# Kernel optimization log

Measured on AMD Instinct MI355X. Metric: run time of the kernel, lower is better.

The kernel has to match this reference:

```python
import jax, jax.numpy as jnp
import numpy as np
import math

B, T, C, H, W = 2, 3, 256, 64, 64   # batch, frames(=n_levels), d_model, feature H/W
M, P = 8, 4                          # n_heads, n_points
DH = C // M                          # dim per head


def conv2d(x, w, b):
    # 3x3 same-padded NCHW conv
    y = jax.lax.conv_general_dilated(x, w, (1, 1), 'SAME',
                                     dimension_numbers=('NCHW', 'OIHW', 'NCHW'))
    return y + b[None, :, None, None]


def setup_inputs() -> dict:
    key = jax.random.key(0)
    ks = jax.random.split(key, 10)
    query = jax.random.normal(ks[0], (B, T, C, H, W), jnp.float32)
    input_flatten = jax.random.normal(ks[1], (B, T, C, H, W), jnp.float32)
    reference_points = jax.random.uniform(ks[2], (B, H * W, T, 2), jnp.float32)
    input_spatial_shapes = jnp.tile(jnp.array([[H, W]], jnp.int32), (T, 1))
    input_level_start_index = jnp.arange(T, dtype=jnp.int32) * (H * W)
    input_padding_mask = jnp.zeros((B, T * H * W), bool)
    flow_forward = jax.random.normal(ks[3], (B, 2, 2, H, W), jnp.float32) * 2.0
    flow_backward = jax.random.normal(ks[4], (B, 2, 2, H, W), jnp.float32) * 2.0
    # conv params
    w_value = jax.random.normal(ks[5], (C, C, 3, 3), jnp.float32) * 0.02
    b_value = jnp.zeros((C,), jnp.float32)
    w_off = jax.random.normal(ks[6], (M * T * P * 2, T * C, 3, 3), jnp.float32) * 1e-3
    # sampling_offsets bias: ring of unit directions scaled by point index (as in _reset_parameters)
    thetas = jnp.arange(M, dtype=jnp.float32) * (2.0 * math.pi / M)
    grid = jnp.stack([jnp.cos(thetas), jnp.sin(thetas)], -1)
    grid = grid / jnp.max(jnp.abs(grid), -1, keepdims=True)
    grid = jnp.tile(grid.reshape(M, 1, 1, 2), (1, T, P, 1)) \
        * (jnp.arange(P, dtype=jnp.float32) + 1.0)[None, None, :, None]
    b_off = grid.reshape(-1)
    w_attn = jax.random.normal(ks[7], (M * T * P, T * C, 3, 3), jnp.float32) * 1e-3
    b_attn = jnp.zeros((M * T * P,), jnp.float32)
    w_out = jax.random.normal(ks[8], (C, C, 3, 3), jnp.float32) * 0.02
    b_out = jnp.zeros((C,), jnp.float32)
    return dict(query=query, reference_points=reference_points, input_flatten=input_flatten,
                input_spatial_shapes=input_spatial_shapes,
                input_level_start_index=input_level_start_index,
                input_padding_mask=input_padding_mask,
                flow_forward=flow_forward, flow_backward=flow_backward,
                w_value=w_value, b_value=b_value, w_off=w_off, b_off=b_off,
                w_attn=w_attn, b_attn=b_attn, w_out=w_out, b_out=b_out)


def ms_deform_attn(value, loc, attn):
    # value: (B, T*H*W, M, DH); loc in [0,1]: (B, Lq, M, T, P, 2); attn: (B, Lq, M, T, P)
    Lq = loc.shape[1]
    val = value.reshape(B, T, H * W, M, DH).transpose(0, 1, 3, 2, 4)  # (B,T,M,HW,DH)
    # grid_sample semantics, align_corners=False, zero padding
    x = loc[..., 0] * W - 0.5
    y = loc[..., 1] * H - 0.5
    x0 = jnp.floor(x); y0 = jnp.floor(y)
    wx = x - x0; wy = y - y0
    x0i = x0.astype(jnp.int32); y0i = y0.astype(jnp.int32)

    def tr(a):  # (B,Lq,M,T,P) -> (B,T,M,Lq*P)
        return jnp.transpose(a, (0, 3, 2, 1, 4)).reshape(B, T, M, Lq * P)

    acc = jnp.zeros((B, T, M, Lq * P, DH), value.dtype)
    for dx, dy, wgt in ((0, 0, (1 - wx) * (1 - wy)), (1, 0, wx * (1 - wy)),
                        (0, 1, (1 - wx) * wy), (1, 1, wx * wy)):
        ix = x0i + dx; iy = y0i + dy
        valid = (ix >= 0) & (ix < W) & (iy >= 0) & (iy < H)
        idx = tr(jnp.clip(iy, 0, H - 1) * W + jnp.clip(ix, 0, W - 1))
        g = jnp.take_along_axis(val, idx[..., None], axis=3)  # (B,T,M,Lq*P,DH)
        acc = acc + g * tr(wgt * valid)[..., None]
    acc = acc.reshape(B, T, M, Lq, P, DH)
    return jnp.einsum('ntmqpd,nqmtp->nqmd', acc, attn).reshape(B, Lq, M * DH)


def reference(query, reference_points, input_flatten, input_spatial_shapes,
              input_level_start_index, input_padding_mask, flow_forward, flow_backward,
              w_value, b_value, w_off, b_off, w_attn, b_attn, w_out, b_out):
    bs, t, c, h, w = query.shape
    value = conv2d(input_flatten.reshape(bs * t, c, h, w), w_value, b_value).reshape(bs, t, c, h, w)
    off = conv2d(query.reshape(bs, t * c, h, w), w_off, b_off)    # (bs, M*T*P*2, h, w)
    attn = conv2d(query.reshape(bs, t * c, h, w), w_attn, b_attn)  # (bs, M*T*P, h, w)

    # flatten to (bs, t*h*w, c) as in torch: flatten(3).transpose(2,3)
    value = value.reshape(bs, t, c, h * w).transpose(0, 1, 3, 2).reshape(bs, t * h * w, c)
    value = jnp.where(input_padding_mask[..., None], 0.0, value)
    value = value.reshape(bs, t * h * w, M, c // M)

    off = off.reshape(bs, -1, h * w).transpose(0, 2, 1).reshape(bs, h * w, M, t, P, 2)
    # flow-guided offsets: level 0 <- backward flow(1->0), level 1 <- zero, level 2 <- forward flow(1->2)
    flow_stack = jnp.stack([flow_backward[:, 0], jnp.zeros_like(flow_forward[:, 1]),
                            flow_forward[:, 1]], axis=2)            # (bs,2,t,h,w)
    flow = flow_stack.reshape(bs, 2, t, h * w).transpose(0, 3, 2, 1)  # (bs,hw,t,2)
    off = off + flow[:, :, None, :, None, :]

    attn = attn.reshape(bs, -1, h * w).transpose(0, 2, 1).reshape(bs, h * w, M, t * P)
    attn = jax.nn.softmax(attn, -1).reshape(bs, h * w, M, t, P)

    normalizer = jnp.stack([input_spatial_shapes[:, 1], input_spatial_shapes[:, 0]], -1).astype(off.dtype)
    loc = reference_points[:, :, None, :, None, :] + off / normalizer[None, None, None, :, None, :]

    out = ms_deform_attn(value, loc, attn)               # (bs, hw, c)
    out = out.reshape(bs, h, w, c).transpose(0, 3, 1, 2)  # (bs, c, h, w)
    return conv2d(out, w_out, b_out)
```

## Files before the change

kernel.cpp:

```cpp
#include <hip/hip_runtime.h>


#define HW_SZ 4096

typedef __attribute__((ext_vector_type(8))) short short8;
typedef __attribute__((ext_vector_type(4))) float f32x4;

__device__ __forceinline__ unsigned short f2bf(float f) {
    union { float f; unsigned u; } v; v.f = f;
    unsigned u = v.u;
    unsigned r = (u + 0x7FFFu + ((u >> 16) & 1u)) >> 16;
    return (unsigned short)r;
}
__device__ __forceinline__ float bf2f(unsigned short h) {
    union { unsigned u; float f; } v; v.u = ((unsigned)h) << 16;
    return v.f;
}

__device__ __forceinline__ void gld16(const void* g, void* l) {
    __builtin_amdgcn_global_load_lds(
        (const __attribute__((address_space(1))) unsigned*)g,
        (__attribute__((address_space(3))) unsigned*)l, 16, 0, 0);
}

__device__ __forceinline__ void repack2(
    int g, const float* __restrict__ w0, const float* __restrict__ w1,
    int split, int Cout, int Cin, unsigned short* __restrict__ out, int OBp)
{
    int lg = g & 3; int rest = g >> 2;
    int KB = Cin >> 5;
    int kb = rest % KB; int oc = rest / KB;
    int ob = oc >> 4, l16 = oc & 15;
    if (oc >= Cout) {
        uint4 z; z.x = z.y = z.z = z.w = 0u;
        #pragma unroll
        for (int tap = 0; tap < 9; ++tap)
            *(uint4*)(out + (((size_t)tap * OBp + ob) * KB + kb) * 512 + (lg * 16 + l16) * 8) = z;
        return;
    }
    const float* src = (oc < split)
        ? (w0 + ((size_t)oc * Cin + kb * 32 + lg * 8) * 9)
        : (w1 + ((size_t)(oc - split) * Cin + kb * 32 + lg * 8) * 9);
    float v[8][9];
    #pragma unroll
    for (int i = 0; i < 8; ++i)
        #pragma unroll
        for (int t = 0; t < 9; ++t)
            v[i][t] = src[i * 9 + t];
    #pragma unroll
    for (int tap = 0; tap < 9; ++tap) {
        unsigned p[4];
        #pragma unroll
        for (int j = 0; j < 4; ++j)
            p[j] = (unsigned)f2bf(v[2 * j][tap]) | ((unsigned)f2bf(v[2 * j + 1][tap]) << 16);
        uint4 o; o.x = p[0]; o.y = p[1]; o.z = p[2]; o.w = p[3];
        *(uint4*)(out + (((size_t)tap * OBp + ob) * KB + kb) * 512 + (lg * 16 + l16) * 8) = o;
    }
}

__global__ __launch_bounds__(256) void prep_fused(
    const float* __restrict__ vin_src, const float* __restrict__ qin_src,
    unsigned short* __restrict__ vdst, unsigned short* __restrict__ qdst,
    const float* __restrict__ w_value, const float* __restrict__ w_off,
    const float* __restrict__ w_attn, const float* __restrict__ w_out,
    const float* __restrict__ b_off, const float* __restrict__ b_attn,
    unsigned short* __restrict__ wpk_v, unsigned short* __restrict__ wpk_q,
    unsigned short* __restrict__ wpk_o, float* __restrict__ qbias,
    float* __restrict__ zbuf)
{
    int bid = blockIdx.x;
    if (bid < 6144) {
        int y = bid & 63, z = bid >> 6;
        const float* in; unsigned short* out; int Cin, img, kb;
        if (z < 48) { img = z >> 3; kb = z & 7; in = vin_src; out = vdst; Cin = 256; }
        else { int h = z - 48; img = h / 24; kb = h % 24; in = qin_src; out = qdst; Cin = 768; }
        __shared__ float s[32][65];
        int t = threadIdx.x;
        int x = t & 63, ic4 = t >> 6;
        const float* ip = in + ((size_t)img * Cin + kb * 32) * HW_SZ + y * 64;
        #pragma unroll
        for (int i = 0; i < 8; ++i) {
            int icl = ic4 * 8 + i;
            s[icl][x] = ip[(size_t)icl * HW_SZ + x];
        }
        __syncthreads();
        int p = t >> 2, h4 = t & 3;
        unsigned v[4];
        #pragma unroll
        for (int j = 0; j < 4; ++j) {
            unsigned lo = f2bf(s[h4 * 8 + 2 * j][p]);
            unsigned hi = f2bf(s[h4 * 8 + 2 * j + 1][p]);
            v[j] = lo | (hi << 16);
        }
        uint4 o; o.x = v[0]; o.y = v[1]; o.z = v[2]; o.w = v[3];
        *(uint4*)(out + ((size_t)img * HW_SZ + y * 64 + p) * Cin + kb * 32 + h4 * 8) = o;
    } else {
        int g = (bid - 6144) * 256 + threadIdx.x;
        if (g < 8192) {
            repack2(g, w_value, w_value, 256, 256, 256, wpk_v, 16);
        } else if (g < 45056) {
            repack2(g - 8192, w_off, w_attn, 192, 288, 768, wpk_q, 24);
        } else if (g < 53248) {
            repack2(g - 45056, w_out, w_out, 256, 256, 256, wpk_o, 16);
        } else {
            int i = g - 53248;
            if (i < 16) zbuf[i] = 0.f;
            if (i < 384) {
                float v = 0.f;
                if (i < 192) v = b_off[i]; else if (i < 288) v = b_attn[i - 192];
                qbias[i] = v;
            }
        }
    }
}

__device__ __forceinline__ void conv_core(
    const unsigned short* __restrict__ gin,
    const unsigned short* __restrict__ wpk,
    const float* __restrict__ bias,
    const unsigned short* __restrict__ zbuf,
    void* __restrict__ outp,
    int Cin, int KB, int OBp, int Cout, int mb, int y0, int outmode, int img,
    unsigned short* sbuf)
{
    const int tid = threadIdx.x;
    const int wv = tid >> 6, lane = tid & 63;
    const int l16 = lane & 15, lg = lane >> 4;
    const int obBase = mb * 8 + wv * 2;

    const unsigned short* sptr[4];
    int okk[4];
    #pragma unroll
    for (int i = 0; i < 4; ++i) {
        int ii = 4 * i + wv;
        int r = ii * 64 + lane;
        sptr[i] = zbuf; okk[i] = 0;
        if (ii < 13 && r < 792) {
            int rr = r / 264;
            int rem = r - rr * 264;
            int icg = rem / 66;
            int cc = rem - icg * 66;
            int gy = y0 - 1 + rr, gx = cc - 1;
            if ((unsigned)gy < 64u && (unsigned)gx < 64u) {
                sptr[i] = gin + ((size_t)(gy * 64 + gx)) * Cin + icg * 8;
                okk[i] = 1;
            }
        }
    }

    f32x4 acc[2][4];
    #pragma unroll
    for (int a = 0; a < 2; ++a)
        #pragma unroll
        for (int b = 0; b < 4; ++b)
            acc[a][b] = (f32x4){0.f, 0.f, 0.f, 0.f};

    auto stage = [&](int kb, unsigned short* sb) {
        #pragma unroll
        for (int i = 0; i < 4; ++i) {
            int ii = 4 * i + wv;
            int r = ii * 64 + lane;
            if (ii < 13 && r < 792) {
                const unsigned short* s = sptr[i] + (okk[i] ? (size_t)kb * 32 : 0);
                gld16(s, sb + (size_t)ii * 64 * 8);
            }
        }
    };

    short8 afr[3][2];
    auto ldA = [&](int kb, int tap, int slot) {
        const unsigned short* wp =
            wpk + (((size_t)tap * OBp + obBase) * KB + kb) * 512;
        #pragma unroll
        for (int ob = 0; ob < 2; ++ob)
            afr[slot][ob] = *(const short8*)(wp + (size_t)ob * KB * 512 + lane * 8);
    };

    short8 bfrb[2][4];
    auto ldB = [&](const unsigned short* cb, int tap, int buf) {
        const int ky = tap / 3, kx = tap % 3;
        #pragma unroll
        for (int pt = 0; pt < 4; ++pt)
            bfrb[buf][pt] = *(const short8*)(cb + (ky * 264 + lg * 66 + kx + pt * 16 + l16) * 8);
    };

    stage(0, sbuf);
    ldA(0, 0, 0); ldA(0, 1, 1); ldA(0, 2, 2);
    for (int kb = 0; kb < KB; ++kb) {
        __syncthreads();
        if (kb + 1 < KB) stage(kb + 1, sbuf + ((kb + 1) & 1) * 6336);
        const unsigned short* cb = sbuf + (kb & 1) * 6336;
        const int kn = (kb + 1 < KB) ? kb + 1 : kb;
        ldB(cb, 0, 0);
        #pragma unroll
        for (int tap = 0; tap < 9; ++tap) {
            const int slot = tap % 3;
            if (tap < 8) ldB(cb, tap + 1, (tap + 1) & 1);
            #pragma unroll
            for (int ob = 0; ob < 2; ++ob)
                #pragma unroll
                for (int pt = 0; pt < 4; ++pt)
                    acc[ob][pt] = __builtin_amdgcn_mfma_f32_16x16x32_bf16(
                        afr[slot][ob], bfrb[tap & 1][pt], acc[ob][pt], 0, 0, 0);
            if (tap < 6) ldA(kb, tap + 3, slot);
            else         ldA(kn, tap - 6, slot);
        }
    }

    if (outmode == 2) {
        float* outf = (float*)outp + (size_t)img * 256 * HW_SZ + (size_t)y0 * 64;
        #pragma unroll
        for (int ob = 0; ob < 2; ++ob) {
            int obg = obBase + ob;
            #pragma unroll
            for (int r = 0; r < 4; ++r) {
                int oc = obg * 16 + lg * 4 + r;
                float bv = bias[oc];
                #pragma unroll
                for (int pt = 0; pt < 4; ++pt)
                    outf[(size_t)oc * HW_SZ + pt * 16 + l16] = acc[ob][pt][r] + bv;
            }
        }
    } else {
        __syncthreads();
        float* s_ep = (float*)sbuf + wv * 1088;
        for (int ob = 0; ob < 2; ++ob) {
            int obg = obBase + ob;
            if (obg * 16 >= Cout) continue;
            #pragma unroll
            for (int r = 0; r < 4; ++r) {
                float bv = bias ? bias[obg * 16 + lg * 4 + r] : 0.f;
                #pragma unroll
                for (int pt = 0; pt < 4; ++pt)
                    s_ep[(pt * 16 + l16) * 17 + lg * 4 + r] = acc[ob][pt][r] + bv;
            }
            size_t pxg = (size_t)img * HW_SZ + (size_t)y0 * 64 + lane;
            if (outmode == 1) {
                float* op = (float*)outp + pxg * 288 + obg * 16;
                #pragma unroll
                for (int jj = 0; jj < 4; ++jj) {
                    float4 t4;
                    t4.x = s_ep[lane * 17 + jj * 4 + 0];
                    t4.y = s_ep[lane * 17 + jj * 4 + 1];
                    t4.z = s_ep[lane * 17 + jj * 4 + 2];
                    t4.w = s_ep[lane * 17 + jj * 4 + 3];
                    *(float4*)(op + jj * 4) = t4;
                }
            } else {
                unsigned short* op = (unsigned short*)outp + pxg * 256 + obg * 16;
                unsigned v[8];
                #pragma unroll
                for (int j = 0; j < 8; ++j) {
                    unsigned lo = f2bf(s_ep[lane * 17 + 2 * j]);
                    unsigned hi = f2bf(s_ep[lane * 17 + 2 * j + 1]);
                    v[j] = lo | (hi << 16);
                }
                uint4 o0; o0.x = v[0]; o0.y = v[1]; o0.z = v[2]; o0.w = v[3];
                uint4 o1; o1.x = v[4]; o1.y = v[5]; o1.z = v[6]; o1.w = v[7];
                *(uint4*)(op) = o0;
                *(uint4*)(op + 8) = o1;
            }
        }
    }
}

__global__ __launch_bounds__(256, 2) void conv_main(
    int ybase,
    const unsigned short* __restrict__ vin, const unsigned short* __restrict__ wv_,
    const float* __restrict__ bv, unsigned short* __restrict__ vout,
    const unsigned short* __restrict__ qin, const unsigned short* __restrict__ wq_,
    const float* __restrict__ bq, float* __restrict__ qout,
    const unsigned short* __restrict__ zbuf)
{
    __shared__ __align__(16) unsigned short sbuf[2 * 6336];
    int g, y0;
    if (ybase < 0) {
        int xcd = blockIdx.x & 7, idx = blockIdx.x >> 3;
        if (xcd < 6) {
            if (idx < 64) { g = xcd; y0 = idx; }
            else if (idx < 112) {
                int v = xcd * 48 + (idx - 64);
                g = 6 + (v >> 6); y0 = v & 63;
            } else {
                return;
            }
        } else {
            int v = 288 + (xcd - 6) * 240 + idx;
            g = 6 + (v >> 6); y0 = v & 63;
        }
    } else {
        g = ybase + blockIdx.y;
        y0 = blockIdx.x;
    }
    if (g < 6) {
        int img = g / 3, mb = g - img * 3;
        conv_core(qin + (size_t)img * HW_SZ * 768, wq_, bq, zbuf, (void*)qout,
                  768, 24, 24, 288, mb, y0, 1, img, sbuf);
    } else {
        int h = g - 6; int img = h >> 1, mb = h & 1;
        conv_core(vin + (size_t)img * HW_SZ * 256, wv_, bv, zbuf, (void*)vout,
                  256, 8, 16, 256, mb, y0, 0, img, sbuf);
    }
}

__global__ __launch_bounds__(256, 2) void conv_out_k(
    const unsigned short* __restrict__ din, const unsigned short* __restrict__ wo_,
    const float* __restrict__ bo, float* __restrict__ outp,
    const unsigned short* __restrict__ zbuf)
{
    __shared__ __align__(16) unsigned short sbuf[2 * 6336];
    int xcd = blockIdx.x & 7, idx = blockIdx.x >> 3;
    int g = xcd >> 1;
    int y0 = (xcd & 1) * 32 + idx;
    int img = g >> 1, mb = g & 1;
    conv_core(din + (size_t)img * HW_SZ * 256, wo_, bo, zbuf, (void*)outp,
              256, 8, 16, 256, mb, y0, 2, img, sbuf);
}

__global__ __launch_bounds__(256) void deform_kernel(
    const unsigned short* __restrict__ value_bf,
    const float* __restrict__ qout,
    const float* __restrict__ refp,
    const float* __restrict__ flow_fwd,
    const float* __restrict__ flow_bwd,
    unsigned short* __restrict__ dout)
{
    int gid = blockIdx.x * 256 + threadIdx.x;
    int d8 = gid & 3;
    int m = (gid >> 2) & 7;
    int q = (gid >> 5) & 4095;
    int b = gid >> 17;

    size_t bq = (size_t)b * HW_SZ + q;
    const float* qbase = qout + bq * 288;
    const float* al = qbase + 192 + m * 12;

    float lg[12];
    float mx = -1e30f;
    #pragma unroll
    for (int i = 0; i < 12; i++) { lg[i] = al[i]; mx = fmaxf(mx, lg[i]); }
    float s = 0.f;
    #pragma unroll
    for (int i = 0; i < 12; i++) { lg[i] = __expf(lg[i] - mx); s += lg[i]; }
    float inv = 1.f / s;

    const float* op = qbase + m * 24;
    const float* rp = refp + bq * 6;

    float acc[8];
    #pragma unroll
    for (int i = 0; i < 8; ++i) acc[i] = 0.f;

    #pragma unroll
    for (int t = 0; t < 3; t++) {
        float fx = 0.f, fy = 0.f;
        if (t == 0) {
            fx = flow_bwd[((b * 2 + 0) * 2 + 0) * HW_SZ + q];
            fy = flow_bwd[((b * 2 + 0) * 2 + 1) * HW_SZ + q];
        } else if (t == 2) {
            fx = flow_fwd[((b * 2 + 1) * 2 + 0) * HW_SZ + q];
            fy = flow_fwd[((b * 2 + 1) * 2 + 1) * HW_SZ + q];
        }
        float rx = rp[t * 2 + 0], ry = rp[t * 2 + 1];
        const unsigned short* vb =
            value_bf + (size_t)(b * 3 + t) * (HW_SZ * 256) + m * 32 + d8 * 8;
        #pragma unroll
        for (int pp = 0; pp < 4; pp++) {
            float ox = op[t * 8 + pp * 2 + 0] + fx;
            float oy = op[t * 8 + pp * 2 + 1] + fy;
            float aw = lg[t * 4 + pp] * inv;
            float x = rx * 64.f + ox - 0.5f;
            float y = ry * 64.f + oy - 0.5f;
            float x0f = floorf(x), y0f = floorf(y);
            float wx = x - x0f, wy = y - y0f;
            int x0 = (int)x0f, y0 = (int)y0f;
            int x1 = x0 + 1, y1 = y0 + 1;
            bool vx0 = (x0 >= 0) & (x0 < 64), vx1 = (x1 >= 0) & (x1 < 64);
            bool vy0 = (y0 >= 0) & (y0 < 64), vy1 = (y1 >= 0) & (y1 < 64);
            int cx0 = min(max(x0, 0), 63), cx1 = min(max(x1, 0), 63);
            int cy0 = min(max(y0, 0), 63), cy1 = min(max(y1, 0), 63);
            float w00 = (1.f - wx) * (1.f - wy) * ((vx0 & vy0) ? 1.f : 0.f) * aw;
            float w10 = wx * (1.f - wy) * ((vx1 & vy0) ? 1.f : 0.f) * aw;
            float w01 = (1.f - wx) * wy * ((vx0 & vy1) ? 1.f : 0.f) * aw;
            float w11 = wx * wy * ((vx1 & vy1) ? 1.f : 0.f) * aw;
            short8 v00 = *(const short8*)(vb + (cy0 * 64 + cx0) * 256);
            short8 v10 = *(const short8*)(vb + (cy0 * 64 + cx1) * 256);
            short8 v01 = *(const short8*)(vb + (cy1 * 64 + cx0) * 256);
            short8 v11 = *(const short8*)(vb + (cy1 * 64 + cx1) * 256);
            #pragma unroll
            for (int i = 0; i < 8; ++i) {
                acc[i] += w00 * bf2f((unsigned short)v00[i])
                        + w10 * bf2f((unsigned short)v10[i])
                        + w01 * bf2f((unsigned short)v01[i])
                        + w11 * bf2f((unsigned short)v11[i]);
            }
        }
    }
    unsigned pk[4];
    #pragma unroll
    for (int j = 0; j < 4; ++j)
        pk[j] = (unsigned)f2bf(acc[2 * j]) | ((unsigned)f2bf(acc[2 * j + 1]) << 16);
    uint4 o; o.x = pk[0]; o.y = pk[1]; o.z = pk[2]; o.w = pk[3];
    *(uint4*)(dout + bq * 256 + m * 32 + d8 * 8) = o;
}

extern "C" void kernel_launch(void* const* d_in, const int* in_sizes, int n_in,
                              void* d_out, int out_size, void* d_ws, size_t ws_size,
                              hipStream_t stream) {
    const float* query   = (const float*)d_in[0];
    const float* refp    = (const float*)d_in[1];
    const float* inflat  = (const float*)d_in[2];
    const float* flowf   = (const float*)d_in[6];
    const float* flowb   = (const float*)d_in[7];
    const float* w_value = (const float*)d_in[8];
    const float* b_value = (const float*)d_in[9];
    const float* w_off   = (const float*)d_in[10];
    const float* b_off   = (const float*)d_in[11];
    const float* w_attn  = (const float*)d_in[12];
    const float* b_attn  = (const float*)d_in[13];
    const float* w_out   = (const float*)d_in[14];
    const float* b_out   = (const float*)d_in[15];

    char* ws = (char*)d_ws;
    unsigned short* wpk_v    = (unsigned short*)(ws);
    unsigned short* wpk_q    = (unsigned short*)(ws + 1179648);
    unsigned short* wpk_o    = (unsigned short*)(ws + 6488064);
    float*          qbias    = (float*)(ws + 7667712);
    float*          zbuf     = (float*)(ws + 7669248);
    unsigned short* value_bf = (unsigned short*)(ws + 7669760);
    unsigned short* qin_bf   = (unsigned short*)(ws + 20252672);
    unsigned short* vin_bf   = (unsigned short*)(ws + 32835584);

    const bool big = ws_size >= 54855680ull;
    float* qout = big ? (float*)(ws + 45418496)
                      : (float*)(ws + 32835584);
    unsigned short* dout_bf = big
        ? (unsigned short*)(ws + 1179648)
        : (unsigned short*)(ws + 42272768);

    prep_fused<<<dim3(6354), dim3(256), 0, stream>>>(
        inflat, query, vin_bf, qin_bf,
        w_value, w_off, w_attn, w_out, b_off, b_attn,
        wpk_v, wpk_q, wpk_o, qbias, zbuf);

    if (big) {
        conv_main<<<dim3(1920), dim3(256), 0, stream>>>(
            -1, vin_bf, wpk_v, b_value, value_bf, qin_bf, wpk_q, qbias, qout,
            (const unsigned short*)zbuf);
    } else {
        conv_main<<<dim3(64, 12), dim3(256), 0, stream>>>(
            6, vin_bf, wpk_v, b_value, value_bf, qin_bf, wpk_q, qbias, qout,
            (const unsigned short*)zbuf);
        conv_main<<<dim3(64, 6), dim3(256), 0, stream>>>(
            0, vin_bf, wpk_v, b_value, value_bf, qin_bf, wpk_q, qbias, qout,
            (const unsigned short*)zbuf);
    }

    deform_kernel<<<dim3(1024), dim3(256), 0, stream>>>(
        value_bf, qout, refp, flowf, flowb, dout_bf);

    conv_out_k<<<dim3(256), dim3(256), 0, stream>>>(
        dout_bf, wpk_o, b_out, (float*)d_out, (const unsigned short*)zbuf);
}
```

Measured before the change: 269.9 us.

## Retile convolutions to two output rows and one oc-block per wave

```diff
diff --git a/kernel.cpp b/kernel.cpp
--- a/kernel.cpp
+++ b/kernel.cpp
@@ -120,27 +120,27 @@
     const float* __restrict__ bias,
     const unsigned short* __restrict__ zbuf,
     void* __restrict__ outp,
-    int Cin, int KB, int OBp, int Cout, int mb, int y0, int outmode, int img,
+    int Cin, int KB, int OBp, int Cout, int mb4, int yp, int outmode, int img,
     unsigned short* sbuf)
 {
     const int tid = threadIdx.x;
     const int wv = tid >> 6, lane = tid & 63;
     const int l16 = lane & 15, lg = lane >> 4;
-    const int obBase = mb * 8 + wv * 2;
-
-    const unsigned short* sptr[4];
-    int okk[4];
-    #pragma unroll
-    for (int i = 0; i < 4; ++i) {
+    const int obg = mb4 * 4 + wv;
+
+    const unsigned short* sptr[5];
+    int okk[5];
+    #pragma unroll
+    for (int i = 0; i < 5; ++i) {
         int ii = 4 * i + wv;
         int r = ii * 64 + lane;
         sptr[i] = zbuf; okk[i] = 0;
-        if (ii < 13 && r < 792) {
+        if (ii < 17 && r < 1056) {
             int rr = r / 264;
             int rem = r - rr * 264;
             int icg = rem / 66;
             int cc = rem - icg * 66;
-            int gy = y0 - 1 + rr, gx = cc - 1;
+            int gy = yp * 2 - 1 + rr, gx = cc - 1;
             if ((unsigned)gy < 64u && (unsigned)gx < 64u) {
                 sptr[i] = gin + ((size_t)(gy * 64 + gx)) * Cin + icg * 8;
                 okk[i] = 1;
@@ -148,48 +148,47 @@
         }
     }
 
-    f32x4 acc[2][4];
-    #pragma unroll
-    for (int a = 0; a < 2; ++a)
-        #pragma unroll
-        for (int b = 0; b < 4; ++b)
-            acc[a][b] = (f32x4){0.f, 0.f, 0.f, 0.f};
+    f32x4 acc[8];
+    #pragma unroll
+    for (int a = 0; a < 8; ++a)
+        acc[a] = (f32x4){0.f, 0.f, 0.f, 0.f};
 
     auto stage = [&](int kb, unsigned short* sb) {
         #pragma unroll
-        for (int i = 0; i < 4; ++i) {
+        for (int i = 0; i < 5; ++i) {
             int ii = 4 * i + wv;
             int r = ii * 64 + lane;
-            if (ii < 13 && r < 792) {
+            if (ii < 17 && r < 1056) {
                 const unsigned short* s = sptr[i] + (okk[i] ? (size_t)kb * 32 : 0);
                 gld16(s, sb + (size_t)ii * 64 * 8);
             }
         }
     };
 
-    short8 afr[3][2];
+    short8 afr[3];
     auto ldA = [&](int kb, int tap, int slot) {
         const unsigned short* wp =
-            wpk + (((size_t)tap * OBp + obBase) * KB + kb) * 512;
-        #pragma unroll
-        for (int ob = 0; ob < 2; ++ob)
-            afr[slot][ob] = *(const short8*)(wp + (size_t)ob * KB * 512 + lane * 8);
+            wpk + (((size_t)tap * OBp + obg) * KB + kb) * 512;
+        afr[slot] = *(const short8*)(wp + lane * 8);
     };
 
-    short8 bfrb[2][4];
+    short8 bfrb[2][8];
     auto ldB = [&](const unsigned short* cb, int tap, int buf) {
         const int ky = tap / 3, kx = tap % 3;
         #pragma unroll
-        for (int pt = 0; pt < 4; ++pt)
-            bfrb[buf][pt] = *(const short8*)(cb + (ky * 264 + lg * 66 + kx + pt * 16 + l16) * 8);
+        for (int r2 = 0; r2 < 2; ++r2)
+            #pragma unroll
+            for (int pt = 0; pt < 4; ++pt)
+                bfrb[buf][r2 * 4 + pt] = *(const short8*)(
+                    cb + ((r2 + ky) * 264 + lg * 66 + kx + pt * 16 + l16) * 8);
     };
 
     stage(0, sbuf);
     ldA(0, 0, 0); ldA(0, 1, 1); ldA(0, 2, 2);
     for (int kb = 0; kb < KB; ++kb) {
         __syncthreads();
-        if (kb + 1 < KB) stage(kb + 1, sbuf + ((kb + 1) & 1) * 6336);
-        const unsigned short* cb = sbuf + (kb & 1) * 6336;
+        if (kb + 1 < KB) stage(kb + 1, sbuf + ((kb + 1) & 1) * 8448);
+        const unsigned short* cb = sbuf + (kb & 1) * 8448;
         const int kn = (kb + 1 < KB) ? kb + 1 : kb;
         ldB(cb, 0, 0);
         #pragma unroll
@@ -197,68 +196,67 @@
             const int slot = tap % 3;
             if (tap < 8) ldB(cb, tap + 1, (tap + 1) & 1);
             #pragma unroll
-            for (int ob = 0; ob < 2; ++ob)
-                #pragma unroll
-                for (int pt = 0; pt < 4; ++pt)
-                    acc[ob][pt] = __builtin_amdgcn_mfma_f32_16x16x32_bf16(
-                        afr[slot][ob], bfrb[tap & 1][pt], acc[ob][pt], 0, 0, 0);
+            for (int a = 0; a < 8; ++a)
+                acc[a] = __builtin_amdgcn_mfma_f32_16x16x32_bf16(
+                    afr[slot], bfrb[tap & 1][a], acc[a], 0, 0, 0);
             if (tap < 6) ldA(kb, tap + 3, slot);
             else         ldA(kn, tap - 6, slot);
         }
     }
 
     if (outmode == 2) {
-        float* outf = (float*)outp + (size_t)img * 256 * HW_SZ + (size_t)y0 * 64;
-        #pragma unroll
-        for (int ob = 0; ob < 2; ++ob) {
-            int obg = obBase + ob;
+        float* outf = (float*)outp + (size_t)img * 256 * HW_SZ;
+        #pragma unroll
+        for (int r2 = 0; r2 < 2; ++r2) {
             #pragma unroll
             for (int r = 0; r < 4; ++r) {
                 int oc = obg * 16 + lg * 4 + r;
                 float bv = bias[oc];
                 #pragma unroll
                 for (int pt = 0; pt < 4; ++pt)
-                    outf[(size_t)oc * HW_SZ + pt * 16 + l16] = acc[ob][pt][r] + bv;
+                    outf[(size_t)oc * HW_SZ + (size_t)(yp * 2 + r2) * 64 + pt * 16 + l16]
+                        = acc[r2 * 4 + pt][r] + bv;
             }
         }
     } else {
         __syncthreads();
         float* s_ep = (float*)sbuf + wv * 1088;
-        for (int ob = 0; ob < 2; ++ob) {
-            int obg = obBase + ob;
-            if (obg * 16 >= Cout) continue;
+        if (obg * 16 < Cout) {
             #pragma unroll
-            for (int r = 0; r < 4; ++r) {
-                float bv = bias ? bias[obg * 16 + lg * 4 + r] : 0.f;
+            for (int r2 = 0; r2 < 2; ++r2) {
                 #pragma unroll
-                for (int pt = 0; pt < 4; ++pt)
-                    s_ep[(pt * 16 + l16) * 17 + lg * 4 + r] = acc[ob][pt][r] + bv;
-            }
-            size_t pxg = (size_t)img * HW_SZ + (size_t)y0 * 64 + lane;
-            if (outmode == 1) {
-                float* op = (float*)outp + pxg * 288 + obg * 16;
-                #pragma unroll
-                for (int jj = 0; jj < 4; ++jj) {
-                    float4 t4;
-                    t4.x = s_ep[lane * 17 + jj * 4 + 0];
-                    t4.y = s_ep[lane * 17 + jj * 4 + 1];
-                    t4.z = s_ep[lane * 17 + jj * 4 + 2];
-                    t4.w = s_ep[lane * 17 + jj * 4 + 3];
-                    *(float4*)(op + jj * 4) = t4;
+                for (int r = 0; r < 4; ++r) {
+                    float bv = bias ? bias[obg * 16 + lg * 4 + r] : 0.f;
+                    #pragma unroll
+                    for (int pt = 0; pt < 4; ++pt)
+                        s_ep[(pt * 16 + l16) * 17 + lg * 4 + r] = acc[r2 * 4 + pt][r] + bv;
                 }
-            } else {
-                unsigned short* op = (unsigned short*)outp + pxg * 256 + obg * 16;
-                unsigned v[8];
-                #pragma unroll
-                for (int j = 0; j < 8; ++j) {
-                    unsigned lo = f2bf(s_ep[lane * 17 + 2 * j]);
-                    unsigned hi = f2bf(s_ep[lane * 17 + 2 * j + 1]);
-                    v[j] = lo | (hi << 16);
+                size_t pxg = (size_t)img * HW_SZ + (size_t)(yp * 2 + r2) * 64 + lane;
+                if (outmode == 1) {
+                    float* op = (float*)outp + pxg * 288 + obg * 16;
+                    #pragma unroll
+                    for (int jj = 0; jj < 4; ++jj) {
+                        float4 t4;
+                        t4.x = s_ep[lane * 17 + jj * 4 + 0];
+                        t4.y = s_ep[lane * 17 + jj * 4 + 1];
+                        t4.z = s_ep[lane * 17 + jj * 4 + 2];
+                        t4.w = s_ep[lane * 17 + jj * 4 + 3];
+                        *(float4*)(op + jj * 4) = t4;
+                    }
+                } else {
+                    unsigned short* op = (unsigned short*)outp + pxg * 256 + obg * 16;
+                    unsigned v[8];
+                    #pragma unroll
+                    for (int j = 0; j < 8; ++j) {
+                        unsigned lo = f2bf(s_ep[lane * 17 + 2 * j]);
+                        unsigned hi = f2bf(s_ep[lane * 17 + 2 * j + 1]);
+                        v[j] = lo | (hi << 16);
+                    }
+                    uint4 o0; o0.x = v[0]; o0.y = v[1]; o0.z = v[2]; o0.w = v[3];
+                    uint4 o1; o1.x = v[4]; o1.y = v[5]; o1.z = v[6]; o1.w = v[7];
+                    *(uint4*)(op) = o0;
+                    *(uint4*)(op + 8) = o1;
                 }
-                uint4 o0; o0.x = v[0]; o0.y = v[1]; o0.z = v[2]; o0.w = v[3];
-                uint4 o1; o1.x = v[4]; o1.y = v[5]; o1.z = v[6]; o1.w = v[7];
-                *(uint4*)(op) = o0;
-                *(uint4*)(op + 8) = o1;
             }
         }
     }
@@ -272,34 +270,36 @@
     const float* __restrict__ bq, float* __restrict__ qout,
     const unsigned short* __restrict__ zbuf)
 {
-    __shared__ __align__(16) unsigned short sbuf[2 * 6336];
-    int g, y0;
+    __shared__ __align__(16) unsigned short sbuf[2 * 8448];
+    int qflag, img, mb4, yp;
     if (ybase < 0) {
         int xcd = blockIdx.x & 7, idx = blockIdx.x >> 3;
-        if (xcd < 6) {
-            if (idx < 64) { g = xcd; y0 = idx; }
-            else if (idx < 112) {
-                int v = xcd * 48 + (idx - 64);
-                g = 6 + (v >> 6); y0 = v & 63;
+        if (xcd < 6 && idx < 64) {
+            qflag = 1; mb4 = xcd; img = idx >> 5; yp = idx & 31;
+        } else {
+            int v;
+            if (xcd < 6) {
+                if (idx >= 112) return;
+                v = xcd * 48 + (idx - 64);
             } else {
-                return;
-            }
-        } else {
-            int v = 288 + (xcd - 6) * 240 + idx;
-            g = 6 + (v >> 6); y0 = v & 63;
+                v = 288 + (xcd - 6) * 240 + idx;
+            }
+            qflag = 0;
+            int gv = v >> 5;
+            img = gv >> 2; mb4 = gv & 3; yp = v & 31;
         }
     } else {
-        g = ybase + blockIdx.y;
-        y0 = blockIdx.x;
-    }
-    if (g < 6) {
-        int img = g / 3, mb = g - img * 3;
+        int g = ybase + blockIdx.y;
+        yp = blockIdx.x;
+        if (g < 12) { qflag = 1; img = g / 6; mb4 = g % 6; }
+        else { qflag = 0; int h = g - 12; img = h >> 2; mb4 = h & 3; }
+    }
+    if (qflag) {
         conv_core(qin + (size_t)img * HW_SZ * 768, wq_, bq, zbuf, (void*)qout,
-                  768, 24, 24, 288, mb, y0, 1, img, sbuf);
+                  768, 24, 24, 288, mb4, yp, 1, img, sbuf);
     } else {
-        int h = g - 6; int img = h >> 1, mb = h & 1;
         conv_core(vin + (size_t)img * HW_SZ * 256, wv_, bv, zbuf, (void*)vout,
-                  256, 8, 16, 256, mb, y0, 0, img, sbuf);
+                  256, 8, 16, 256, mb4, yp, 0, img, sbuf);
     }
 }
 
@@ -308,13 +308,11 @@
     const float* __restrict__ bo, float* __restrict__ outp,
     const unsigned short* __restrict__ zbuf)
 {
-    __shared__ __align__(16) unsigned short sbuf[2 * 6336];
-    int xcd = blockIdx.x & 7, idx = blockIdx.x >> 3;
-    int g = xcd >> 1;
-    int y0 = (xcd & 1) * 32 + idx;
-    int img = g >> 1, mb = g & 1;
+    __shared__ __align__(16) unsigned short sbuf[2 * 8448];
+    int xcd = blockIdx.x & 7, yp = blockIdx.x >> 3;
+    int img = xcd >> 2, mb4 = xcd & 3;
     conv_core(din + (size_t)img * HW_SZ * 256, wo_, bo, zbuf, (void*)outp,
-              256, 8, 16, 256, mb, y0, 2, img, sbuf);
+              256, 8, 16, 256, mb4, yp, 2, img, sbuf);
 }
 
 __global__ __launch_bounds__(256) void deform_kernel(
@@ -325,7 +323,8 @@
     const float* __restrict__ flow_bwd,
     unsigned short* __restrict__ dout)
 {
-    int gid = blockIdx.x * 256 + threadIdx.x;
+    int xcd = blockIdx.x & 7, idx = blockIdx.x >> 3;
+    int gid = (xcd * 128 + idx) * 256 + threadIdx.x;
     int d8 = gid & 3;
     int m = (gid >> 2) & 7;
     int q = (gid >> 5) & 4095;
@@ -448,10 +447,10 @@
             -1, vin_bf, wpk_v, b_value, value_bf, qin_bf, wpk_q, qbias, qout,
             (const unsigned short*)zbuf);
     } else {
-        conv_main<<<dim3(64, 12), dim3(256), 0, stream>>>(
-            6, vin_bf, wpk_v, b_value, value_bf, qin_bf, wpk_q, qbias, qout,
+        conv_main<<<dim3(32, 24), dim3(256), 0, stream>>>(
+            12, vin_bf, wpk_v, b_value, value_bf, qin_bf, wpk_q, qbias, qout,
             (const unsigned short*)zbuf);
-        conv_main<<<dim3(64, 6), dim3(256), 0, stream>>>(
+        conv_main<<<dim3(32, 12), dim3(256), 0, stream>>>(
             0, vin_bf, wpk_v, b_value, value_bf, qin_bf, wpk_q, qbias, qout,
             (const unsigned short*)zbuf);
     }
```

Result: no change. 274.2 us (+1.6%).
